# Kernel optimization log

Measured on AMD Instinct MI355X. Metric: run time of the kernel, lower is better.

The kernel has to match this reference:

```python
import jax, jax.numpy as jnp
import numpy as np

# Product manifold layout: [Lorentz(DH) | Sphere(DS) | Euclidean(DE)]
DH, DS, DE = 64, 32, 32
GAMMA = 12.0
EPS = 1e-6


def _split(x):
    return x[..., :DH], x[..., DH:DH + DS], x[..., DH + DS:]


def _minkowski_inner(x, y):
    # <x,y>_L = -x0*y0 + sum_i xi*yi over last dim
    return -x[..., 0] * y[..., 0] + jnp.sum(x[..., 1:] * y[..., 1:], axis=-1)


def _project_entities(x):
    # Place raw gaussian points onto the product manifold (mimics sample_uniform + projection).
    xh, xs, xe = _split(x)
    rest = xh[..., 1:]
    x0 = jnp.sqrt(1.0 + jnp.sum(rest * rest, axis=-1, keepdims=True))
    xh = jnp.concatenate([x0, rest], axis=-1)          # on hyperboloid <x,x>_L = -1
    xs = xs / jnp.linalg.norm(xs, axis=-1, keepdims=True)  # on unit sphere
    return jnp.concatenate([xh, xs, xe], axis=-1)


def _translate(h, r):
    # translated = exp_map(h, proj_tangent(h, r)) per manifold component
    hh, hs, he = _split(h)
    rh, rs, re = _split(r)
    # Lorentz: proj_tangent v = r + <h,r>_L h ; exp_map = cosh(|v|)h + sinh(|v|)v/|v|
    ip = _minkowski_inner(hh, rh)[..., None]
    vh = rh + ip * hh
    vn = jnp.sqrt(jnp.clip(_minkowski_inner(vh, vh), EPS, None))[..., None]
    th = jnp.cosh(vn) * hh + jnp.sinh(vn) * (vh / vn)
    # Sphere: proj_tangent v = r - <h,r> h ; exp_map = cos(|v|)h + sin(|v|)v/|v|
    ips = jnp.sum(hs * rs, axis=-1, keepdims=True)
    vs = rs - ips * hs
    vns = jnp.clip(jnp.linalg.norm(vs, axis=-1, keepdims=True), EPS, None)
    ts = jnp.cos(vns) * hs + jnp.sin(vns) * (vs / vns)
    # Euclidean: exp_map = h + r
    te = he + re
    return th, ts, te


def _dist_all(th, ts, te, ent):
    # Pairwise geodesic distance (B,E) against all entities, per component, combined L2.
    eh, es, ee = _split(ent)
    sign = jnp.concatenate([-jnp.ones((1,), th.dtype), jnp.ones((DH - 1,), th.dtype)])
    inner_h = (th * sign) @ eh.T                                   # (B,E) Minkowski inner
    dh = jnp.arccosh(jnp.clip(-inner_h, 1.0 + EPS, None))          # clamped acosh
    inner_s = ts @ es.T
    ds = jnp.arccos(jnp.clip(inner_s, -1.0 + EPS, 1.0 - EPS))      # clamped acos
    de2 = jnp.clip(
        jnp.sum(te * te, -1)[:, None] + jnp.sum(ee * ee, -1)[None, :] - 2.0 * (te @ ee.T),
        0.0, None)
    return jnp.sqrt(dh * dh + ds * ds + de2 + EPS)


def setup_inputs() -> dict:
    key = jax.random.key(0)
    k1, k2, k3, k4 = jax.random.split(key, 4)
    E, R, B, D = 200000, 500, 64, 128
    ent_emb = _project_entities(jax.random.normal(k1, (E, D), jnp.float32) * 0.5)
    rel_emb = jax.random.normal(k2, (R, D), jnp.float32) * 0.1
    h_ids = jax.random.randint(k3, (B,), 0, E)
    r_ids = jax.random.randint(k4, (B,), 0, R)
    return {"h_ids": h_ids, "r_ids": r_ids, "ent_emb": ent_emb, "rel_emb": rel_emb}


def reference(h_ids, r_ids, ent_emb, rel_emb):
    # score_all_tails: (B, num_entities) scores = gamma - dist(translate(h, r), all_entities)
    h = ent_emb[h_ids]          # (B, D)
    r = rel_emb[r_ids]          # (B, D)
    th, ts, te = _translate(h, r)
    dist = _dist_all(th, ts, te, ent_emb)  # (B, E)
    return GAMMA - dist
```

## Files before the change

kernel.cpp:

```cpp
#include <hip/hip_runtime.h>
#include <math.h>

#define DHYP 64
#define DSPH 32
#define DEUC 32
#define DTOT 128
#define GAMMA_C 12.0f
#define EPS_C 1e-6f

typedef __attribute__((ext_vector_type(8))) __bf16 bf16x8;
typedef __attribute__((ext_vector_type(4))) float f32x4;

__global__ void rie_build_queries(const int* __restrict__ h_ids,
                                  const int* __restrict__ r_ids,
                                  const float* __restrict__ ent,
                                  const float* __restrict__ rel,
                                  bf16x8* __restrict__ ah_tab,
                                  bf16x8* __restrict__ al_tab,
                                  float* __restrict__ te2v, int B) {
  int b = blockIdx.x * blockDim.x + threadIdx.x;
  if (b >= B) return;
  const float* __restrict__ h = ent + (long long)h_ids[b] * DTOT;
  const float* __restrict__ r = rel + (long long)r_ids[b] * DTOT;

  float tq[DTOT];

  float ip = -h[0] * r[0];
#pragma unroll
  for (int k = 1; k < DHYP; ++k) ip = fmaf(h[k], r[k], ip);
  float v0 = fmaf(ip, h[0], r[0]);
  float mvv = -v0 * v0;
#pragma unroll
  for (int k = 1; k < DHYP; ++k) {
    float v = fmaf(ip, h[k], r[k]);
    mvv = fmaf(v, v, mvv);
  }
  float vn = sqrtf(fmaxf(mvv, EPS_C));
  float ch = coshf(vn);
  float sh = sinhf(vn) / vn;
#pragma unroll
  for (int k = 0; k < DHYP; ++k) {
    float v = fmaf(ip, h[k], r[k]);
    float th = ch * h[k] + sh * v;
    tq[k] = (k == 0) ? -th : th;
  }

  float ips = 0.0f;
#pragma unroll
  for (int j = 0; j < DSPH; ++j) ips = fmaf(h[DHYP + j], r[DHYP + j], ips);
  float nv = 0.0f;
#pragma unroll
  for (int j = 0; j < DSPH; ++j) {
    float v = fmaf(-ips, h[DHYP + j], r[DHYP + j]);
    nv = fmaf(v, v, nv);
  }
  float vns = fmaxf(sqrtf(nv), EPS_C);
  float cs = cosf(vns);
  float sn = sinf(vns) / vns;
#pragma unroll
  for (int j = 0; j < DSPH; ++j) {
    float v = fmaf(-ips, h[DHYP + j], r[DHYP + j]);
    tq[DHYP + j] = cs * h[DHYP + j] + sn * v;
  }

  float te2 = 0.0f;
#pragma unroll
  for (int j = 0; j < DEUC; ++j) {
    float t = h[DHYP + DSPH + j] + r[DHYP + DSPH + j];
    tq[DHYP + DSPH + j] = t;
    te2 = fmaf(t, t, te2);
  }
  te2v[b] = te2;

  const int mt = b >> 4;
  const int lmod = b & 15;
#pragma unroll
  for (int c = 0; c < 4; ++c) {
#pragma unroll
    for (int g = 0; g < 4; ++g) {
      bf16x8 Ah, Al;
#pragma unroll
      for (int j = 0; j < 8; ++j) {
        float x = tq[32 * c + 8 * g + j];
        __bf16 hx = (__bf16)x;
        Ah[j] = hx;
        Al[j] = (__bf16)(x - (float)hx);
      }
      int idx = (c * 4 + mt) * 64 + g * 16 + lmod;
      ah_tab[idx] = Ah;
      al_tab[idx] = Al;
    }
  }
}

__device__ __forceinline__ float fast_acos(float x) {
  float ax = fabsf(x);
  float p = fmaf(ax, -0.0187293f, 0.0742610f);
  p = fmaf(p, ax, -0.2121144f);
  p = fmaf(p, ax, 1.5707288f);
  float r = sqrtf(fmaxf(1.0f - ax, 0.0f)) * p;
  return (x < 0.0f) ? (3.14159265358979f - r) : r;
}

__device__ __forceinline__ float fast_acosh(float x) {
  float t = x + sqrtf(fmaxf(fmaf(x, x, -1.0f), 0.0f));
  return 0.69314718055995f * __log2f(t);
}

__device__ __forceinline__ void split8(const f32x4& lo, const f32x4& hi,
                                       bf16x8& Bh, bf16x8& Bl) {
#pragma unroll
  for (int j = 0; j < 4; ++j) {
    float x = lo[j];
    __bf16 hx = (__bf16)x;
    Bh[j] = hx;
    Bl[j] = (__bf16)(x - (float)hx);
    float y = hi[j];
    __bf16 hy = (__bf16)y;
    Bh[j + 4] = hy;
    Bl[j + 4] = (__bf16)(y - (float)hy);
  }
}

__device__ __forceinline__ void mt_step(const bf16x8* tab_lds, int base,
                                        const bf16x8& Bh, const bf16x8& Bl,
                                        f32x4& acc) {
  bf16x8 Ah = tab_lds[base];
  bf16x8 Al = tab_lds[base + 1024];
  acc = __builtin_amdgcn_mfma_f32_16x16x32_bf16(Ah, Bh, acc, 0, 0, 0);
  acc = __builtin_amdgcn_mfma_f32_16x16x32_bf16(Al, Bh, acc, 0, 0, 0);
  acc = __builtin_amdgcn_mfma_f32_16x16x32_bf16(Ah, Bl, acc, 0, 0, 0);
}

__global__ __launch_bounds__(256, 4) void rie_dist_mfma(
    const float* __restrict__ ent, const bf16x8* __restrict__ ah_tab,
    const float* __restrict__ te2v, float* __restrict__ out, int E) {
  __shared__ bf16x8 tab_lds[2048];

  const int lane = threadIdx.x & 63;
  const int wave = threadIdx.x >> 6;
  const int e0 = (blockIdx.x * 4 + wave) * 16;
  const int lmod = lane & 15;
  const int lgrp = lane >> 4;

  const float* __restrict__ erow =
      ent + (long long)(e0 + lmod) * DTOT + 8 * lgrp;
  f32x4 b0a = *reinterpret_cast<const f32x4*>(erow);
  f32x4 b0b = *reinterpret_cast<const f32x4*>(erow + 4);
  f32x4 b1a = *reinterpret_cast<const f32x4*>(erow + 32);
  f32x4 b1b = *reinterpret_cast<const f32x4*>(erow + 36);
  f32x4 b2a = *reinterpret_cast<const f32x4*>(erow + 64);
  f32x4 b2b = *reinterpret_cast<const f32x4*>(erow + 68);
  f32x4 b3a = *reinterpret_cast<const f32x4*>(erow + 96);
  f32x4 b3b = *reinterpret_cast<const f32x4*>(erow + 100);

#pragma unroll
  for (int j = 0; j < 8; ++j)
    tab_lds[threadIdx.x + j * 256] = ah_tab[threadIdx.x + j * 256];
  __syncthreads();

  float ee2 = 0.0f;
#pragma unroll
  for (int j = 0; j < 4; ++j) {
    ee2 = fmaf(b3a[j], b3a[j], ee2);
    ee2 = fmaf(b3b[j], b3b[j], ee2);
  }
  ee2 += __shfl_xor(ee2, 16);
  ee2 += __shfl_xor(ee2, 32);

  const f32x4 z = {0.f, 0.f, 0.f, 0.f};
  f32x4 aH0 = z, aH1 = z, aH2 = z, aH3 = z;
  f32x4 aS0 = z, aS1 = z, aS2 = z, aS3 = z;
  f32x4 aE0 = z, aE1 = z, aE2 = z, aE3 = z;

  {
    bf16x8 Bh, Bl;
    split8(b0a, b0b, Bh, Bl);
    mt_step(tab_lds, (0 * 4 + 0) * 64 + lane, Bh, Bl, aH0);
    mt_step(tab_lds, (0 * 4 + 1) * 64 + lane, Bh, Bl, aH1);
    mt_step(tab_lds, (0 * 4 + 2) * 64 + lane, Bh, Bl, aH2);
    mt_step(tab_lds, (0 * 4 + 3) * 64 + lane, Bh, Bl, aH3);
  }
  {
    bf16x8 Bh, Bl;
    split8(b1a, b1b, Bh, Bl);
    mt_step(tab_lds, (1 * 4 + 0) * 64 + lane, Bh, Bl, aH0);
    mt_step(tab_lds, (1 * 4 + 1) * 64 + lane, Bh, Bl, aH1);
    mt_step(tab_lds, (1 * 4 + 2) * 64 + lane, Bh, Bl, aH2);
    mt_step(tab_lds, (1 * 4 + 3) * 64 + lane, Bh, Bl, aH3);
  }
  {
    bf16x8 Bh, Bl;
    split8(b2a, b2b, Bh, Bl);
    mt_step(tab_lds, (2 * 4 + 0) * 64 + lane, Bh, Bl, aS0);
    mt_step(tab_lds, (2 * 4 + 1) * 64 + lane, Bh, Bl, aS1);
    mt_step(tab_lds, (2 * 4 + 2) * 64 + lane, Bh, Bl, aS2);
    mt_step(tab_lds, (2 * 4 + 3) * 64 + lane, Bh, Bl, aS3);
  }
  {
    bf16x8 Bh, Bl;
    split8(b3a, b3b, Bh, Bl);
    mt_step(tab_lds, (3 * 4 + 0) * 64 + lane, Bh, Bl, aE0);
    mt_step(tab_lds, (3 * 4 + 1) * 64 + lane, Bh, Bl, aE1);
    mt_step(tab_lds, (3 * 4 + 2) * 64 + lane, Bh, Bl, aE2);
    mt_step(tab_lds, (3 * 4 + 3) * 64 + lane, Bh, Bl, aE3);
  }

#define EPI(MT, AH, AS, AE)                                                   \
  {                                                                           \
    const f32x4 t2 =                                                          \
        *reinterpret_cast<const f32x4*>(te2v + MT * 16 + 4 * lgrp);           \
    _Pragma("unroll") for (int r = 0; r < 4; ++r) {                           \
      float x = fmaxf(-AH[r], 1.0f + EPS_C);                                  \
      float dh = fast_acosh(x);                                               \
      float yv = fminf(fmaxf(AS[r], -1.0f + EPS_C), 1.0f - EPS_C);            \
      float dsv = fast_acos(yv);                                              \
      float de2 = fmaxf(t2[r] + ee2 - 2.0f * AE[r], 0.0f);                    \
      float dist = sqrtf(fmaf(dh, dh, fmaf(dsv, dsv, de2 + EPS_C)));          \
      out[(long long)(MT * 16 + 4 * lgrp + r) * E + e0 + lmod] =              \
          GAMMA_C - dist;                                                     \
    }                                                                         \
  }
  EPI(0, aH0, aS0, aE0);
  EPI(1, aH1, aS1, aE1);
  EPI(2, aH2, aS2, aE2);
  EPI(3, aH3, aS3, aE3);
#undef EPI
}

extern "C" void kernel_launch(void* const* d_in, const int* in_sizes, int n_in,
                              void* d_out, int out_size, void* d_ws,
                              size_t ws_size, hipStream_t stream) {
  const int* h_ids = (const int*)d_in[0];
  const int* r_ids = (const int*)d_in[1];
  const float* ent = (const float*)d_in[2];
  const float* rel = (const float*)d_in[3];
  float* out = (float*)d_out;

  const int B = in_sizes[0];
  const int E = in_sizes[2] / DTOT;

  bf16x8* ah_tab = (bf16x8*)d_ws;
  bf16x8* al_tab = ah_tab + 1024;
  float* te2v = (float*)((char*)d_ws + 32768);

  rie_build_queries<<<1, 64, 0, stream>>>(h_ids, r_ids, ent, rel, ah_tab,
                                          al_tab, te2v, B);

  const int blocks = (E + 63) / 64;
  rie_dist_mfma<<<blocks, 256, 0, stream>>>(ent, ah_tab, te2v, out, E);
}
```

Before: 210.5 us.

## Parallelize query translation across wave lanes and split fragment packing into separate kernel

The single-block, one-thread-per-query prologue kernel is replaced by two kernels. The first assigns one 64-lane wave per query, with each lane holding two dimensions and wave shuffle reductions computing the inner products and norms. The second packs the fp32 query rows into bf16 hi/lo MFMA fragment tables. This removes a long serial per-thread loop with a 128-float register array, at the cost of one extra kernel launch and a round trip through global memory for the query rows.

```diff
diff --git a/kernel.cpp b/kernel.cpp
--- a/kernel.cpp
+++ b/kernel.cpp
@@ -11,85 +11,87 @@
 typedef __attribute__((ext_vector_type(8))) __bf16 bf16x8;
 typedef __attribute__((ext_vector_type(4))) float f32x4;
 
-__global__ void rie_build_queries(const int* __restrict__ h_ids,
-                                  const int* __restrict__ r_ids,
-                                  const float* __restrict__ ent,
-                                  const float* __restrict__ rel,
-                                  bf16x8* __restrict__ ah_tab,
-                                  bf16x8* __restrict__ al_tab,
-                                  float* __restrict__ te2v, int B) {
-  int b = blockIdx.x * blockDim.x + threadIdx.x;
+__device__ __forceinline__ float wsum64(float x) {
+#pragma unroll
+  for (int off = 1; off < 64; off <<= 1) x += __shfl_xor(x, off);
+  return x;
+}
+
+__global__ void rie_translate(const int* __restrict__ h_ids,
+                              const int* __restrict__ r_ids,
+                              const float* __restrict__ ent,
+                              const float* __restrict__ rel,
+                              float* __restrict__ qrows,
+                              float* __restrict__ te2v, int B) {
+  const int lane = threadIdx.x & 63;
+  const int wave = threadIdx.x >> 6;
+  const int b = blockIdx.x * (blockDim.x >> 6) + wave;
   if (b >= B) return;
+
   const float* __restrict__ h = ent + (long long)h_ids[b] * DTOT;
   const float* __restrict__ r = rel + (long long)r_ids[b] * DTOT;
-
-  float tq[DTOT];
-
-  float ip = -h[0] * r[0];
-#pragma unroll
-  for (int k = 1; k < DHYP; ++k) ip = fmaf(h[k], r[k], ip);
-  float v0 = fmaf(ip, h[0], r[0]);
-  float mvv = -v0 * v0;
-#pragma unroll
-  for (int k = 1; k < DHYP; ++k) {
-    float v = fmaf(ip, h[k], r[k]);
-    mvv = fmaf(v, v, mvv);
-  }
+  const float h1 = h[lane], h2 = h[64 + lane];
+  const float r1 = r[lane], r2 = r[64 + lane];
+
+  float ip = wsum64(lane == 0 ? -h1 * r1 : h1 * r1);
+  float v = fmaf(ip, h1, r1);
+  float mvv = wsum64(lane == 0 ? -v * v : v * v);
   float vn = sqrtf(fmaxf(mvv, EPS_C));
   float ch = coshf(vn);
   float sh = sinhf(vn) / vn;
-#pragma unroll
-  for (int k = 0; k < DHYP; ++k) {
-    float v = fmaf(ip, h[k], r[k]);
-    float th = ch * h[k] + sh * v;
-    tq[k] = (k == 0) ? -th : th;
-  }
-
-  float ips = 0.0f;
-#pragma unroll
-  for (int j = 0; j < DSPH; ++j) ips = fmaf(h[DHYP + j], r[DHYP + j], ips);
-  float nv = 0.0f;
-#pragma unroll
-  for (int j = 0; j < DSPH; ++j) {
-    float v = fmaf(-ips, h[DHYP + j], r[DHYP + j]);
-    nv = fmaf(v, v, nv);
-  }
+  float th = ch * h1 + sh * v;
+  float q1 = (lane == 0) ? -th : th;
+
+  const bool is_s = lane < 32;
+  float ips = wsum64(is_s ? h2 * r2 : 0.0f);
+  float vs = fmaf(-ips, h2, r2);
+  float nv = wsum64(is_s ? vs * vs : 0.0f);
   float vns = fmaxf(sqrtf(nv), EPS_C);
   float cs = cosf(vns);
   float sn = sinf(vns) / vns;
-#pragma unroll
-  for (int j = 0; j < DSPH; ++j) {
-    float v = fmaf(-ips, h[DHYP + j], r[DHYP + j]);
-    tq[DHYP + j] = cs * h[DHYP + j] + sn * v;
-  }
-
-  float te2 = 0.0f;
-#pragma unroll
-  for (int j = 0; j < DEUC; ++j) {
-    float t = h[DHYP + DSPH + j] + r[DHYP + DSPH + j];
-    tq[DHYP + DSPH + j] = t;
-    te2 = fmaf(t, t, te2);
-  }
-  te2v[b] = te2;
-
-  const int mt = b >> 4;
-  const int lmod = b & 15;
-#pragma unroll
-  for (int c = 0; c < 4; ++c) {
-#pragma unroll
-    for (int g = 0; g < 4; ++g) {
-      bf16x8 Ah, Al;
-#pragma unroll
-      for (int j = 0; j < 8; ++j) {
-        float x = tq[32 * c + 8 * g + j];
-        __bf16 hx = (__bf16)x;
-        Ah[j] = hx;
-        Al[j] = (__bf16)(x - (float)hx);
-      }
-      int idx = (c * 4 + mt) * 64 + g * 16 + lmod;
-      ah_tab[idx] = Ah;
-      al_tab[idx] = Al;
+  float ts = cs * h2 + sn * vs;
+
+  float te = h2 + r2;
+  float te2 = wsum64(is_s ? 0.0f : te * te);
+  float q2 = is_s ? ts : te;
+
+  qrows[b * DTOT + lane] = q1;
+  qrows[b * DTOT + 64 + lane] = q2;
+  if (lane == 0) te2v[b] = te2;
+}
+
+__global__ void rie_pack_frags(const float* __restrict__ qrows,
+                               bf16x8* __restrict__ ah_tab,
+                               bf16x8* __restrict__ al_tab) {
+  const int t = threadIdx.x;
+#pragma unroll
+  for (int i = 0; i < 4; ++i) {
+    const int idx = t + i * 256;
+    const int cmt = idx >> 6;
+    const int c = cmt >> 2;
+    const int mt = cmt & 3;
+    const int lane = idx & 63;
+    const int lmod = lane & 15;
+    const int g = lane >> 4;
+    const int row = mt * 16 + lmod;
+    const int k0 = 32 * c + 8 * g;
+    const float* __restrict__ src = qrows + row * DTOT + k0;
+    const f32x4 a = *reinterpret_cast<const f32x4*>(src);
+    const f32x4 bb = *reinterpret_cast<const f32x4*>(src + 4);
+    bf16x8 Ah, Al;
+#pragma unroll
+    for (int j = 0; j < 4; ++j) {
+      float x = a[j];
+      __bf16 hx = (__bf16)x;
+      Ah[j] = hx;
+      Al[j] = (__bf16)(x - (float)hx);
+      float y = bb[j];
+      __bf16 hy = (__bf16)y;
+      Ah[j + 4] = hy;
+      Al[j + 4] = (__bf16)(y - (float)hy);
     }
+    ah_tab[idx] = Ah;
+    al_tab[idx] = Al;
   }
 }
 
@@ -243,9 +245,11 @@
   bf16x8* ah_tab = (bf16x8*)d_ws;
   bf16x8* al_tab = ah_tab + 1024;
   float* te2v = (float*)((char*)d_ws + 32768);
-
-  rie_build_queries<<<1, 64, 0, stream>>>(h_ids, r_ids, ent, rel, ah_tab,
-                                          al_tab, te2v, B);
+  float* qrows = te2v + 256;
+
+  rie_translate<<<(B * 64 + 255) / 256, 256, 0, stream>>>(h_ids, r_ids, ent,
+                                                          rel, qrows, te2v, B);
+  rie_pack_frags<<<1, 256, 0, stream>>>(qrows, ah_tab, al_tab);
 
   const int blocks = (E + 63) / 64;
   rie_dist_mfma<<<blocks, 256, 0, stream>>>(ent, ah_tab, te2v, out, E);
```

Result: faster. 182.2 us, median of 2 (-13.4%).
